# Kernel tuning notes

Hardware: AMD Instinct MI355X
Metric: run time of the kernel (lower is better)

Reference implementation:

```python
import jax, jax.numpy as jnp
import numpy as np

EMB = 512
HEADS = 8
HEAD_DIM = EMB // HEADS


def setup_inputs() -> dict:
    key = jax.random.key(0)
    ks = jax.random.split(key, 9)
    s = 1.0 / np.sqrt(EMB)
    return {
        "x": jax.random.normal(ks[0], (4, 2048, EMB), dtype=jnp.float32),
        "Wq": jax.random.uniform(ks[1], (EMB, EMB), jnp.float32, -s, s),
        "bq": jax.random.uniform(ks[2], (EMB,), jnp.float32, -s, s),
        "Wk": jax.random.uniform(ks[3], (EMB, EMB), jnp.float32, -s, s),
        "bk": jax.random.uniform(ks[4], (EMB,), jnp.float32, -s, s),
        "Wv": jax.random.uniform(ks[5], (EMB, EMB), jnp.float32, -s, s),
        "bv": jax.random.uniform(ks[6], (EMB,), jnp.float32, -s, s),
        "Wp": jax.random.uniform(ks[7], (EMB, EMB), jnp.float32, -s, s),
        "bp": jax.random.uniform(ks[8], (EMB,), jnp.float32, -s, s),
    }


def _split_heads(t):
    b, n, _ = t.shape
    return t.reshape(b, n, HEADS, HEAD_DIM).transpose(0, 2, 1, 3)  # b h n d


def reference(x, Wq, bq, Wk, bk, Wv, bv, Wp, bp):
    q = _split_heads(x @ Wq.T + bq)
    k = _split_heads(x @ Wk.T + bk)
    v = _split_heads(x @ Wv.T + bv)
    energy = jnp.einsum("bhqd,bhkd->bhqk", q, k)
    # NOTE: original applies softmax to UNSCALED logits, then divides probs by sqrt(emb)
    att = jax.nn.softmax(energy, axis=-1) / jnp.sqrt(jnp.float32(EMB))
    out = jnp.einsum("bhqk,bhkd->bhqd", att, v)
    b, h, n, d = out.shape
    out = out.transpose(0, 2, 1, 3).reshape(b, n, h * d)
    return out @ Wp.T + bp
```

## Files before the change

### kernel.cpp

```cpp
#include <hip/hip_runtime.h>
#include <math.h>
#include <stdint.h>

#define SEQ  2048
#define LOG2E 1.4426950408889634f

typedef __attribute__((ext_vector_type(4))) float f32x4;
typedef __attribute__((ext_vector_type(16))) float f32x16;
typedef __attribute__((ext_vector_type(8))) short bf16x8;

template <int V> struct IC { static constexpr int value = V; };

__device__ __forceinline__ unsigned packbf(float a, float b) {
    return __builtin_amdgcn_perm(__float_as_uint(b) + 0x8000u,
                                 __float_as_uint(a) + 0x8000u, 0x07060302u);
}

__global__ __launch_bounds__(256) void cvt_kernel(
    const float* __restrict__ x,  const float* __restrict__ wq,
    const float* __restrict__ wk, const float* __restrict__ wv,
    const float* __restrict__ wp,
    unsigned short* __restrict__ xb,  unsigned short* __restrict__ wqb,
    unsigned short* __restrict__ wkb, unsigned short* __restrict__ wvb,
    unsigned short* __restrict__ wpb)
{
    const int c = blockIdx.x * 256 + threadIdx.x;
    const float* s;
    unsigned short* d;
    int off;
    if (c < 524288) {
        s = x; d = xb; off = c;
    } else {
        const int cc = c - 524288;
        const int wsel = cc >> 15;
        off = cc & 32767;
        s = wsel == 0 ? wq : wsel == 1 ? wk : wsel == 2 ? wv : wp;
        d = wsel == 0 ? wqb : wsel == 1 ? wkb : wsel == 2 ? wvb : wpb;
    }
    const float4* sp = (const float4*)s + (size_t)off * 2;
    const float4 a = sp[0], b = sp[1];
    uint4 p;
    p.x = packbf(a.x, a.y); p.y = packbf(a.z, a.w);
    p.z = packbf(b.x, b.y); p.w = packbf(b.z, b.w);
    *((uint4*)d + off) = p;
}

__global__ __launch_bounds__(256, 3) void qkv_kernel(
    const unsigned short* __restrict__ xb, const unsigned short* __restrict__ wqb,
    const unsigned short* __restrict__ wkb, const unsigned short* __restrict__ wvb,
    const float* __restrict__ bq, const float* __restrict__ bk,
    const float* __restrict__ bv,
    unsigned short* __restrict__ Qw, unsigned short* __restrict__ Kw,
    unsigned short* __restrict__ VTw)
{
    __shared__ __align__(16) unsigned short smem[8192];
    unsigned short* As = smem;
    unsigned short* Bs = smem + 4096;

    const int t = threadIdx.x;
    const int w = t >> 6, lane = t & 63, quad = (t >> 4) & 3, l15 = t & 15;
    const int wr = w >> 1, wc = w & 1;
    const int m0 = blockIdx.y * 128;
    const int n0 = blockIdx.x * 128;
    const int which = n0 >> 9;
    const unsigned short* wbase = which == 0 ? wqb : (which == 1 ? wkb : wvb);
    const int nrow = n0 & 511;

    const int ar = t >> 2, akq = t & 3;
    const unsigned short* ax = xb + (size_t)(m0 + ar) * 512 + akq * 8;
    const unsigned short* bx = wbase + (size_t)(nrow + ar) * 512 + akq * 8;
    const int lws = (ar & 15) | (akq << 4);
    const int off0 = (ar >> 4) * 512 + lws * 8;
    const int off1 = off0 + 4 * 512;

    f32x4 acc[4][4];
#pragma unroll
    for (int mt = 0; mt < 4; ++mt)
#pragma unroll
        for (int nt = 0; nt < 4; ++nt) acc[mt][nt] = (f32x4){0.f, 0.f, 0.f, 0.f};

    uint4 ra0, ra1, rb0, rb1;
    auto loadt = [&](int k0) {
        ra0 = *(const uint4*)(ax + k0);
        ra1 = *(const uint4*)(ax + 32768 + k0);
        rb0 = *(const uint4*)(bx + k0);
        rb1 = *(const uint4*)(bx + 32768 + k0);
    };
    auto writet = [&]() {
        *(uint4*)(As + off0) = ra0;
        *(uint4*)(As + off1) = ra1;
        *(uint4*)(Bs + off0) = rb0;
        *(uint4*)(Bs + off1) = rb1;
    };

    loadt(0);
    auto kloop = [&](auto TRC) {
        constexpr int TR = decltype(TRC)::value;
        for (int ki = 0; ki < 16; ++ki) {
            writet();
            if (ki < 15) loadt((ki + 1) * 32);
            __syncthreads();
            bf16x8 af[4], bfr[4];
#pragma unroll
            for (int mt = 0; mt < 4; ++mt)
                af[mt] = *(const bf16x8*)(As + ((wr * 4 + mt) * 64 + lane) * 8);
#pragma unroll
            for (int nt = 0; nt < 4; ++nt)
                bfr[nt] = *(const bf16x8*)(Bs + ((wc * 4 + nt) * 64 + lane) * 8);
#pragma unroll
            for (int mt = 0; mt < 4; ++mt)
#pragma unroll
                for (int nt = 0; nt < 4; ++nt) {
                    if (TR)
                        acc[mt][nt] = __builtin_amdgcn_mfma_f32_16x16x32_bf16(
                            bfr[nt], af[mt], acc[mt][nt], 0, 0, 0);
                    else
                        acc[mt][nt] = __builtin_amdgcn_mfma_f32_16x16x32_bf16(
                            af[mt], bfr[nt], acc[mt][nt], 0, 0, 0);
                }
            if (ki < 15) __syncthreads();
        }
    };
    if (which < 2) kloop(IC<1>{});
    else           kloop(IC<0>{});

    if (which == 2) {
#pragma unroll
        for (int nt = 0; nt < 4; ++nt) {
            const int n = n0 + wc * 64 + nt * 16 + l15;
            const float bias = bv[n & 511];
            const int h = (n >> 6) & 7, d = n & 63;
#pragma unroll
            for (int mt = 0; mt < 4; ++mt) {
                const int mb = m0 + wr * 64 + mt * 16 + quad * 4;
                const int bi = mb >> 11, ns = mb & 2047;
                const int bhl = bi * 8 + h;
                const f32x4 v = acc[mt][nt];
                uint2 pk;
                pk.x = packbf(v[0] + bias, v[1] + bias);
                pk.y = packbf(v[2] + bias, v[3] + bias);
                const size_t off =
                    ((size_t)(bhl * 32 + (ns >> 6)) * 8 + ((d >> 5) << 2) +
                     ((ns >> 4) & 3)) * 512 +
                    ((d & 31) << 3) + ((ns & 8) << 5) + (ns & 7);
                *(uint2*)(VTw + off) = pk;
            }
        }
    } else {
        const float sc = which ? 1.f : LOG2E;
        const float* bpt = which ? bk : bq;
        unsigned short* base = which ? Kw : Qw;
#pragma unroll
        for (int nt = 0; nt < 4; ++nt) {
            const int nb = n0 + wc * 64 + nt * 16 + quad * 4;
            const f32x4 bvv = *(const f32x4*)(bpt + (nb & 511));
            const int h = (nb >> 6) & 7, d0 = nb & 63;
#pragma unroll
            for (int mt = 0; mt < 4; ++mt) {
                const int nsg = m0 + wr * 64 + mt * 16 + l15;
                const int bi = nsg >> 11, ns = nsg & 2047;
                const int bhl = bi * 8 + h;
                const f32x4 v = acc[mt][nt];
                uint2 pk;
                pk.x = packbf((v[0] + bvv[0]) * sc, (v[1] + bvv[1]) * sc);
                pk.y = packbf((v[2] + bvv[2]) * sc, (v[3] + bvv[3]) * sc);
                const size_t off =
                    ((size_t)(bhl * 64 + (ns >> 5)) * 4 + (d0 >> 4)) * 512 +
                    ((d0 & 8) << 5) + ((ns & 31) << 3) + (d0 & 7);
                *(uint2*)(base + off) = pk;
            }
        }
    }
}

__global__ __launch_bounds__(256, 3) void outproj_kernel(
    const unsigned short* __restrict__ Aw, const unsigned short* __restrict__ wpb,
    const float* __restrict__ bp, float* __restrict__ out)
{
    __shared__ __align__(16) unsigned short smem[6144];
    unsigned short* As = smem;
    unsigned short* Bs = smem + 4096;

    const int t = threadIdx.x;
    const int w = t >> 6, lane = t & 63, quad = (t >> 4) & 3, l15 = t & 15;
    const int wr = w >> 1, wc = w & 1;
    const int m0 = blockIdx.y * 128;
    const int n0 = blockIdx.x * 64;

    const int ar = t >> 2, akq = t & 3;
    const unsigned short* ap = Aw + (size_t)(m0 + ar) * 512 + akq * 8;
    const unsigned short* bx = wpb + (size_t)(n0 + ar) * 512 + akq * 8;
    const int lws = (ar & 15) | (akq << 4);
    const int off0 = (ar >> 4) * 512 + lws * 8;
    const int off1 = off0 + 4 * 512;
    const int boff = (ar >> 4) * 512 + lws * 8;

    f32x4 acc[4][2];
#pragma unroll
    for (int mt = 0; mt < 4; ++mt)
#pragma unroll
        for (int nt = 0; nt < 2; ++nt) acc[mt][nt] = (f32x4){0.f, 0.f, 0.f, 0.f};

    uint4 ra0, ra1, rb0;
    auto loadt = [&](int k0) {
        ra0 = *(const uint4*)(ap + k0);
        ra1 = *(const uint4*)(ap + 32768 + k0);
        rb0 = *(const uint4*)(bx + k0);
    };
    auto writet = [&]() {
        *(uint4*)(As + off0) = ra0;
        *(uint4*)(As + off1) = ra1;
        *(uint4*)(Bs + boff) = rb0;
    };

    loadt(0);
    for (int ki = 0; ki < 16; ++ki) {
        writet();
        if (ki < 15) loadt((ki + 1) * 32);
        __syncthreads();
        bf16x8 af[4], bfr[2];
#pragma unroll
        for (int mt = 0; mt < 4; ++mt)
            af[mt] = *(const bf16x8*)(As + ((wr * 4 + mt) * 64 + lane) * 8);
#pragma unroll
        for (int nt = 0; nt < 2; ++nt)
            bfr[nt] = *(const bf16x8*)(Bs + ((wc * 2 + nt) * 64 + lane) * 8);
#pragma unroll
        for (int mt = 0; mt < 4; ++mt)
#pragma unroll
            for (int nt = 0; nt < 2; ++nt)
                acc[mt][nt] = __builtin_amdgcn_mfma_f32_16x16x32_bf16(
                    af[mt], bfr[nt], acc[mt][nt], 0, 0, 0);
        if (ki < 15) __syncthreads();
    }

#pragma unroll
    for (int nt = 0; nt < 2; ++nt) {
        const int n = n0 + wc * 32 + nt * 16 + l15;
        const float bias = bp[n];
#pragma unroll
        for (int mt = 0; mt < 4; ++mt) {
            const int mb = m0 + wr * 64 + mt * 16 + quad * 4;
            const f32x4 v = acc[mt][nt];
#pragma unroll
            for (int r = 0; r < 4; ++r)
                out[(size_t)(mb + r) * 512 + n] = v[r] + bias;
        }
    }
}

__global__ __launch_bounds__(512, 4) void attn_kernel(
    const unsigned short* __restrict__ Qf, const unsigned short* __restrict__ Kf,
    const unsigned short* __restrict__ Vf, unsigned short* __restrict__ Ow)
{
    __shared__ float cb[8448];
    const int t = threadIdx.x;
    const int w = t >> 6, lane = t & 63;
    const int l31 = lane & 31, hlf = lane >> 5;
    const int qi = w >> 1, jh = w & 1;

    const int bh = blockIdx.x;
    const int qblk = blockIdx.y;
    const int q0 = qblk * 128;

    const unsigned short* Kp = Kf + (size_t)bh * 131072 + (jh * 4) * 512 + lane * 8;
    const unsigned short* Vp = Vf + (size_t)bh * 131072 + lane * 8;

    const int qgg = qblk * 4 + qi;
    const unsigned short* Qp = Qf + ((size_t)(bh * 64 + qgg) * 4) * 512 + lane * 8;
    bf16x8 qf[4];
#pragma unroll
    for (int kt = 0; kt < 4; ++kt)
        qf[kt] = *(const bf16x8*)(Qp + kt * 512);

    f32x16 zero;
#pragma unroll
    for (int r = 0; r < 16; ++r) zero[r] = 0.f;

    float lpart = 0.f;
    f32x16 Ot[2];
    Ot[0] = zero; Ot[1] = zero;

    bf16x8 kc[4];
#pragma unroll
    for (int c = 0; c < 4; ++c)
        kc[c] = *(const bf16x8*)(Kp + c * 512);

    for (int jt = 0; jt < 32; ++jt) {
        bf16x8 vc[4];
#pragma unroll
        for (int dg = 0; dg < 2; ++dg)
#pragma unroll
            for (int p = 0; p < 2; ++p)
                vc[dg * 2 + p] = *(const bf16x8*)(
                    Vp + (size_t)jt * 4096 + (dg * 4 + jh * 2 + p) * 512);

        f32x16 st = zero;
        __builtin_amdgcn_s_setprio(1);
#pragma unroll
        for (int kt = 0; kt < 4; ++kt)
            st = __builtin_amdgcn_mfma_f32_32x32x16_bf16(kc[kt], qf[kt], st, 0, 0, 0);
        __builtin_amdgcn_s_setprio(0);

        const int jn = (jt < 31) ? jt + 1 : 31;
#pragma unroll
        for (int c = 0; c < 4; ++c)
            kc[c] = *(const bf16x8*)(Kp + (size_t)jn * 4096 + c * 512);

#pragma unroll
        for (int r = 0; r < 16; ++r)
            st[r] = __builtin_amdgcn_exp2f(st[r]);
        {
            float s01 = st[0] + st[1],   s23 = st[2] + st[3];
            float s45 = st[4] + st[5],   s67 = st[6] + st[7];
            float s89 = st[8] + st[9],   sAB = st[10] + st[11];
            float sCD = st[12] + st[13], sEF = st[14] + st[15];
            lpart += ((s01 + s23) + (s45 + s67)) + ((s89 + sAB) + (sCD + sEF));
        }

#pragma unroll
        for (int p = 0; p < 2; ++p) {
            const int r0 = p * 8;
            unsigned a0, a1, b0, b1;
            asm("v_cvt_pk_bf16_f32 %0, %1, %2"
                : "=v"(a0) : "v"(st[r0 + 0]), "v"(st[r0 + 1]));
            asm("v_cvt_pk_bf16_f32 %0, %1, %2"
                : "=v"(a1) : "v"(st[r0 + 2]), "v"(st[r0 + 3]));
            asm("v_cvt_pk_bf16_f32 %0, %1, %2"
                : "=v"(b0) : "v"(st[r0 + 4]), "v"(st[r0 + 5]));
            asm("v_cvt_pk_bf16_f32 %0, %1, %2"
                : "=v"(b1) : "v"(st[r0 + 6]), "v"(st[r0 + 7]));
            asm("v_permlane32_swap_b32 %0, %1" : "+v"(a0), "+v"(b0));
            asm("v_permlane32_swap_b32 %0, %1" : "+v"(a1), "+v"(b1));
            union { unsigned u[4]; bf16x8 v; } pb;
            pb.u[0] = a0;
            pb.u[1] = a1;
            pb.u[2] = b0;
            pb.u[3] = b1;
            __builtin_amdgcn_s_setprio(1);
            Ot[0] = __builtin_amdgcn_mfma_f32_32x32x16_bf16(vc[0 + p], pb.v, Ot[0], 0, 0, 0);
            Ot[1] = __builtin_amdgcn_mfma_f32_32x32x16_bf16(vc[2 + p], pb.v, Ot[1], 0, 0, 0);
            __builtin_amdgcn_s_setprio(0);
        }
    }

    if (jh == 1) {
#pragma unroll
        for (int dg = 0; dg < 2; ++dg) {
            const int cidx = (qi * 2 + dg) * 4;
#pragma unroll
            for (int k = 0; k < 4; ++k) {
                float4 v = make_float4(
                    Ot[dg][k * 4 + 0], Ot[dg][k * 4 + 1],
                    Ot[dg][k * 4 + 2], Ot[dg][k * 4 + 3]);
                *(float4*)(cb + (cidx + k) * 256 + lane * 4) = v;
            }
        }
        cb[8192 + qi * 64 + lane] = lpart;
    }
    __syncthreads();
    if (jh == 0) {
        const int bi = bh >> 3, h = bh & 7;
#pragma unroll
        for (int dg = 0; dg < 2; ++dg) {
            const int cidx = (qi * 2 + dg) * 4;
#pragma unroll
            for (int k = 0; k < 4; ++k) {
                const float4 v = *(const float4*)(cb + (cidx + k) * 256 + lane * 4);
                Ot[dg][k * 4 + 0] += v.x;
                Ot[dg][k * 4 + 1] += v.y;
                Ot[dg][k * 4 + 2] += v.z;
                Ot[dg][k * 4 + 3] += v.w;
            }
        }
        float lv = lpart + cb[8192 + qi * 64 + lane];
        lv += __shfl_xor(lv, 32);
        const float inv = 1.0f / (lv * 22.627416997969522f);

        const int ns = q0 + qi * 32 + l31;
        unsigned short* dst = Ow + ((size_t)bi * SEQ + ns) * 512 + h * 64 + hlf * 4;
#pragma unroll
        for (int dg = 0; dg < 2; ++dg)
#pragma unroll
            for (int rb2 = 0; rb2 < 4; ++rb2) {
                uint2 pk;
                pk.x = packbf(Ot[dg][rb2 * 4 + 0] * inv,
                              Ot[dg][rb2 * 4 + 1] * inv);
                pk.y = packbf(Ot[dg][rb2 * 4 + 2] * inv,
                              Ot[dg][rb2 * 4 + 3] * inv);
                *(uint2*)(dst + dg * 32 + rb2 * 8) = pk;
            }
    }
}

extern "C" void kernel_launch(void* const* d_in, const int* in_sizes, int n_in,
                              void* d_out, int out_size, void* d_ws, size_t ws_size,
                              hipStream_t stream)
{
    const float* x  = (const float*)d_in[0];
    const float* Wq = (const float*)d_in[1];
    const float* bq = (const float*)d_in[2];
    const float* Wk = (const float*)d_in[3];
    const float* bk = (const float*)d_in[4];
    const float* Wv = (const float*)d_in[5];
    const float* bv = (const float*)d_in[6];
    const float* Wp = (const float*)d_in[7];
    const float* bp = (const float*)d_in[8];

    unsigned short* ws = (unsigned short*)d_ws;
    unsigned short* Qw  = ws;
    unsigned short* Kw  = Qw + 4194304;
    unsigned short* VTw = Kw + 4194304;
    unsigned short* Owb = VTw + 4194304;
    unsigned short* xb  = Owb;
    unsigned short* wqb = Owb + 4194304;
    unsigned short* wkb = wqb + 262144;
    unsigned short* wvb = wkb + 262144;
    unsigned short* wpb = wvb + 262144;

    cvt_kernel<<<dim3(2560), 256, 0, stream>>>(
        x, Wq, Wk, Wv, Wp, xb, wqb, wkb, wvb, wpb);
    qkv_kernel<<<dim3(12, 64), 256, 0, stream>>>(
        xb, wqb, wkb, wvb, bq, bk, bv, Qw, Kw, VTw);
    attn_kernel<<<dim3(32, 16), 512, 0, stream>>>(Qw, Kw, VTw, Owb);
    outproj_kernel<<<dim3(8, 64), 256, 0, stream>>>(Owb, wpb, bp, (float*)d_out);
}
```

Measured before the change: 163.4 us.

## Software-pipeline QK^T of the next key tile with softmax/PV of current

Unrolls the attention key loop by two and ping-pongs between two score accumulators. The QK^T MFMAs for tile j+1 are issued before the exp2, bf16 pack and PV MFMAs for tile j, so matrix-core and VALU work can overlap. K fragments are now prefetched two tiles ahead. Launch bounds drop from 4 to 2 blocks per CU to leave room for the extra live registers, which may cut occupancy. One redundant QK^T on the clamped last tile is computed and discarded.

```diff
diff --git a/kernel.cpp b/kernel.cpp
--- a/kernel.cpp
+++ b/kernel.cpp
@@ -249,7 +249,66 @@
     }
 }
 
-__global__ __launch_bounds__(512, 4) void attn_kernel(
+#define ATTN_STEP(STC, STN, JT)                                                \
+    do {                                                                       \
+        const int jt_ = (JT);                                                  \
+        bf16x8 vc[4];                                                          \
+        _Pragma("unroll")                                                      \
+        for (int dg = 0; dg < 2; ++dg)                                         \
+            _Pragma("unroll")                                                  \
+            for (int p = 0; p < 2; ++p)                                        \
+                vc[dg * 2 + p] = *(const bf16x8*)(                             \
+                    Vp + (size_t)jt_ * 4096 + (dg * 4 + jh * 2 + p) * 512);    \
+        STN = zero;                                                            \
+        __builtin_amdgcn_s_setprio(1);                                         \
+        _Pragma("unroll")                                                      \
+        for (int kt = 0; kt < 4; ++kt)                                         \
+            STN = __builtin_amdgcn_mfma_f32_32x32x16_bf16(kc[kt], qf[kt],      \
+                                                          STN, 0, 0, 0);       \
+        __builtin_amdgcn_s_setprio(0);                                         \
+        const int jn_ = (jt_ < 30) ? jt_ + 2 : 31;                             \
+        _Pragma("unroll")                                                      \
+        for (int c = 0; c < 4; ++c)                                            \
+            kc[c] = *(const bf16x8*)(Kp + (size_t)jn_ * 4096 + c * 512);       \
+        _Pragma("unroll")                                                      \
+        for (int r = 0; r < 16; ++r)                                           \
+            STC[r] = __builtin_amdgcn_exp2f(STC[r]);                           \
+        {                                                                      \
+            float s01 = STC[0] + STC[1],   s23 = STC[2] + STC[3];              \
+            float s45 = STC[4] + STC[5],   s67 = STC[6] + STC[7];              \
+            float s89 = STC[8] + STC[9],   sAB = STC[10] + STC[11];            \
+            float sCD = STC[12] + STC[13], sEF = STC[14] + STC[15];            \
+            lpart += ((s01 + s23) + (s45 + s67)) + ((s89 + sAB) + (sCD + sEF));\
+        }                                                                      \
+        _Pragma("unroll")                                                      \
+        for (int p = 0; p < 2; ++p) {                                          \
+            const int r0 = p * 8;                                              \
+            unsigned a0, a1, b0, b1;                                           \
+            asm("v_cvt_pk_bf16_f32 %0, %1, %2"                                 \
+                : "=v"(a0) : "v"(STC[r0 + 0]), "v"(STC[r0 + 1]));              \
+            asm("v_cvt_pk_bf16_f32 %0, %1, %2"                                 \
+                : "=v"(a1) : "v"(STC[r0 + 2]), "v"(STC[r0 + 3]));              \
+            asm("v_cvt_pk_bf16_f32 %0, %1, %2"                                 \
+                : "=v"(b0) : "v"(STC[r0 + 4]), "v"(STC[r0 + 5]));              \
+            asm("v_cvt_pk_bf16_f32 %0, %1, %2"                                 \
+                : "=v"(b1) : "v"(STC[r0 + 6]), "v"(STC[r0 + 7]));              \
+            asm("v_permlane32_swap_b32 %0, %1" : "+v"(a0), "+v"(b0));          \
+            asm("v_permlane32_swap_b32 %0, %1" : "+v"(a1), "+v"(b1));          \
+            union { unsigned u[4]; bf16x8 v; } pb;                             \
+            pb.u[0] = a0;                                                      \
+            pb.u[1] = a1;                                                      \
+            pb.u[2] = b0;                                                      \
+            pb.u[3] = b1;                                                      \
+            __builtin_amdgcn_s_setprio(1);                                     \
+            Ot[0] = __builtin_amdgcn_mfma_f32_32x32x16_bf16(vc[0 + p], pb.v,   \
+                                                            Ot[0], 0, 0, 0);   \
+            Ot[1] = __builtin_amdgcn_mfma_f32_32x32x16_bf16(vc[2 + p], pb.v,   \
+                                                            Ot[1], 0, 0, 0);   \
+            __builtin_amdgcn_s_setprio(0);                                     \
+        }                                                                      \
+    } while (0)
+
+__global__ __launch_bounds__(512, 2) void attn_kernel(
     const unsigned short* __restrict__ Qf, const unsigned short* __restrict__ Kf,
     const unsigned short* __restrict__ Vf, unsigned short* __restrict__ Ow)
 {
@@ -286,62 +345,17 @@
     for (int c = 0; c < 4; ++c)
         kc[c] = *(const bf16x8*)(Kp + c * 512);
 
-    for (int jt = 0; jt < 32; ++jt) {
-        bf16x8 vc[4];
-#pragma unroll
-        for (int dg = 0; dg < 2; ++dg)
-#pragma unroll
-            for (int p = 0; p < 2; ++p)
-                vc[dg * 2 + p] = *(const bf16x8*)(
-                    Vp + (size_t)jt * 4096 + (dg * 4 + jh * 2 + p) * 512);
-
-        f32x16 st = zero;
-        __builtin_amdgcn_s_setprio(1);
-#pragma unroll
-        for (int kt = 0; kt < 4; ++kt)
-            st = __builtin_amdgcn_mfma_f32_32x32x16_bf16(kc[kt], qf[kt], st, 0, 0, 0);
-        __builtin_amdgcn_s_setprio(0);
-
-        const int jn = (jt < 31) ? jt + 1 : 31;
-#pragma unroll
-        for (int c = 0; c < 4; ++c)
-            kc[c] = *(const bf16x8*)(Kp + (size_t)jn * 4096 + c * 512);
-
-#pragma unroll
-        for (int r = 0; r < 16; ++r)
-            st[r] = __builtin_amdgcn_exp2f(st[r]);
-        {
-            float s01 = st[0] + st[1],   s23 = st[2] + st[3];
-            float s45 = st[4] + st[5],   s67 = st[6] + st[7];
-            float s89 = st[8] + st[9],   sAB = st[10] + st[11];
-            float sCD = st[12] + st[13], sEF = st[14] + st[15];
-            lpart += ((s01 + s23) + (s45 + s67)) + ((s89 + sAB) + (sCD + sEF));
-        }
-
-#pragma unroll
-        for (int p = 0; p < 2; ++p) {
-            const int r0 = p * 8;
-            unsigned a0, a1, b0, b1;
-            asm("v_cvt_pk_bf16_f32 %0, %1, %2"
-                : "=v"(a0) : "v"(st[r0 + 0]), "v"(st[r0 + 1]));
-            asm("v_cvt_pk_bf16_f32 %0, %1, %2"
-                : "=v"(a1) : "v"(st[r0 + 2]), "v"(st[r0 + 3]));
-            asm("v_cvt_pk_bf16_f32 %0, %1, %2"
-                : "=v"(b0) : "v"(st[r0 + 4]), "v"(st[r0 + 5]));
-            asm("v_cvt_pk_bf16_f32 %0, %1, %2"
-                : "=v"(b1) : "v"(st[r0 + 6]), "v"(st[r0 + 7]));
-            asm("v_permlane32_swap_b32 %0, %1" : "+v"(a0), "+v"(b0));
-            asm("v_permlane32_swap_b32 %0, %1" : "+v"(a1), "+v"(b1));
-            union { unsigned u[4]; bf16x8 v; } pb;
-            pb.u[0] = a0;
-            pb.u[1] = a1;
-            pb.u[2] = b0;
-            pb.u[3] = b1;
-            __builtin_amdgcn_s_setprio(1);
-            Ot[0] = __builtin_amdgcn_mfma_f32_32x32x16_bf16(vc[0 + p], pb.v, Ot[0], 0, 0, 0);
-            Ot[1] = __builtin_amdgcn_mfma_f32_32x32x16_bf16(vc[2 + p], pb.v, Ot[1], 0, 0, 0);
-            __builtin_amdgcn_s_setprio(0);
-        }
+    f32x16 stA = zero, stB = zero;
+#pragma unroll
+    for (int kt = 0; kt < 4; ++kt)
+        stA = __builtin_amdgcn_mfma_f32_32x32x16_bf16(kc[kt], qf[kt], stA, 0, 0, 0);
+#pragma unroll
+    for (int c = 0; c < 4; ++c)
+        kc[c] = *(const bf16x8*)(Kp + 4096 + c * 512);
+
+    for (int jt = 0; jt < 32; jt += 2) {
+        ATTN_STEP(stA, stB, jt);
+        ATTN_STEP(stB, stA, jt + 1);
     }
 
     if (jh == 1) {
```

Measured after the change: 162.9 us. No clear change (-0.3%).
